# Performance work log

Measured on AMD Instinct MI355X. Metric: run time of the kernel, lower is better.

Reference implementation:

```python
import jax, jax.numpy as jnp
import numpy as np

H, C = 8, 16          # heads, per-head dim; hidden = H*C = 128
NEG_SLOPE = 0.2       # GATConv default
EPS = 1e-5            # GraphNorm eps


def setup_inputs() -> dict:
    key = jax.random.key(0)
    ks = iter(jax.random.split(key, 64))
    Np, Na, D, E = 100000, 50000, 128, 500000
    s = 1.0 / np.sqrt(D)

    def w(shape, scale=1.0):
        return jax.random.normal(next(ks), shape, jnp.float32) * scale

    inp = {
        'x_paper': w((Np, D)),
        'x_author': w((Na, D)),
        'edge_writes': jnp.stack([
            jax.random.randint(next(ks), (E,), 0, Na),
            jax.random.randint(next(ks), (E,), 0, Np)]).astype(jnp.int32),
        'edge_cites': jnp.stack([
            jax.random.randint(next(ks), (E,), 0, Np),
            jax.random.randint(next(ks), (E,), 0, Np)]).astype(jnp.int32),
        'W_lin_paper': w((D, 128), s), 'b_lin_paper': jnp.zeros((128,), jnp.float32),
        'W_lin_author': w((D, 128), s), 'b_lin_author': jnp.zeros((128,), jnp.float32),
        'Wsrc_writes': w((128, 128), s), 'Wdst_writes': w((128, 128), s),
        'atts_writes': w((H, C), 0.1), 'attd_writes': w((H, C), 0.1),
        'bias_writes': jnp.zeros((128,), jnp.float32),
        'Wsrc_cites': w((128, 128), s), 'Wdst_cites': w((128, 128), s),
        'atts_cites': w((H, C), 0.1), 'attd_cites': w((H, C), 0.1),
        'bias_cites': jnp.zeros((128,), jnp.float32),
        'gnw_paper': jnp.ones((128,), jnp.float32), 'gnb_paper': jnp.zeros((128,), jnp.float32),
        'gnm_paper': jnp.ones((128,), jnp.float32),
        'gnw_author': jnp.ones((128,), jnp.float32), 'gnb_author': jnp.zeros((128,), jnp.float32),
        'gnm_author': jnp.ones((128,), jnp.float32),
        'W2_paper': w((128, 128), s), 'b2_paper': jnp.zeros((128,), jnp.float32),
        'W2_author': w((128, 128), s), 'b2_author': jnp.zeros((128,), jnp.float32),
    }
    return inp


def _gat(src_emb, dst_emb, ei, Wsrc, Wdst, att_s, att_d, bias, n_dst):
    # PyG GATConv, bipartite input, concat=True, add_self_loops=True (eval / no dropout)
    n_self = min(src_emb.shape[0], n_dst)
    loops = jnp.arange(n_self, dtype=ei.dtype)
    src = jnp.concatenate([ei[0], loops])
    dst = jnp.concatenate([ei[1], loops])
    xs = (src_emb @ Wsrc).reshape(-1, H, C)          # [Ns,H,C]
    xd = (dst_emb @ Wdst).reshape(-1, H, C)          # [Nd,H,C]
    a_s = (xs * att_s).sum(-1)                       # [Ns,H]
    a_d = (xd * att_d).sum(-1)                       # [Nd,H]
    e = jax.nn.leaky_relu(a_s[src] + a_d[dst], NEG_SLOPE)   # [E,H]
    m = jax.ops.segment_max(e, dst, num_segments=n_dst)
    m = jnp.where(jnp.isfinite(m), m, 0.0)           # guard empty segments
    p = jnp.exp(e - m[dst])
    denom = jax.ops.segment_sum(p, dst, num_segments=n_dst)
    alpha = p / (denom[dst] + 1e-16)                 # segment softmax over dst
    msg = xs[src] * alpha[:, :, None]                # [E,H,C]
    out = jax.ops.segment_sum(msg, dst, num_segments=n_dst)  # [Nd,H,C]
    return out.reshape(n_dst, H * C) + bias


def _gnorm(x, w, b, ms):
    mu = x.mean(0)
    o = x - ms * mu
    var = (o * o).mean(0)
    return w * o * jax.lax.rsqrt(var + EPS) + b


def reference(x_paper, x_author, edge_writes, edge_cites,
              W_lin_paper, b_lin_paper, W_lin_author, b_lin_author,
              Wsrc_writes, Wdst_writes, atts_writes, attd_writes, bias_writes,
              Wsrc_cites, Wdst_cites, atts_cites, attd_cites, bias_cites,
              gnw_paper, gnb_paper, gnm_paper, gnw_author, gnb_author, gnm_author,
              W2_paper, b2_paper, W2_author, b2_author):
    emb_p = jax.nn.relu(x_paper @ W_lin_paper + b_lin_paper)
    emb_a = jax.nn.relu(x_author @ W_lin_author + b_lin_author)
    Np = emb_p.shape[0]
    out_p = _gat(emb_a, emb_p, edge_writes, Wsrc_writes, Wdst_writes,
                 atts_writes, attd_writes, bias_writes, Np)
    out_p = out_p + _gat(emb_p, emb_p, edge_cites, Wsrc_cites, Wdst_cites,
                         atts_cites, attd_cites, bias_cites, Np)
    out_a = jnp.zeros((emb_a.shape[0], H * C), x_author.dtype)  # no edge type targets author
    out_p = _gnorm(out_p, gnw_paper, gnb_paper, gnm_paper) @ W2_paper + b2_paper
    out_a = _gnorm(out_a, gnw_author, gnb_author, gnm_author) @ W2_author + b2_author
    return (out_p, out_a)
```

## Files before the change

### kernel.cpp

```cpp
#include <hip/hip_runtime.h>
#include <cstdint>
#include <cstddef>

#define H 8
#define DHID 128
#define BM 64
#define LDST 136
#define NEG_SLOPE 0.2f
#define GN_EPS 1e-5f

#define SCAN_T 256
#define SCAN_I 4

typedef __attribute__((ext_vector_type(8))) short short8;
typedef __attribute__((ext_vector_type(4))) float f32x4;

__device__ __forceinline__ void atomAddF(float* p, float v) {
    __hip_atomic_fetch_add(p, v, __ATOMIC_RELAXED, __HIP_MEMORY_SCOPE_AGENT);
}
__device__ __forceinline__ unsigned short f2bf(float f) {
    uint32_t u = __float_as_uint(f);
    uint32_t r = (u + 0x7FFFu + ((u >> 16) & 1u)) >> 16;
    return (unsigned short)r;
}
__device__ __forceinline__ uint32_t pack2bf(float lo, float hi) {
    return (uint32_t)f2bf(lo) | ((uint32_t)f2bf(hi) << 16);
}
__device__ __forceinline__ float bflo(uint32_t v) { return __uint_as_float(v << 16); }
__device__ __forceinline__ float bfhi(uint32_t v) { return __uint_as_float(v & 0xFFFF0000u); }

struct PrepHist {
    const float *Wlp, *Wsc, *Wla, *Wsw, *W2p;
    const float *Wdw, *adw, *asc_, *Wdc, *adc_, *asw_;
    unsigned short *WlinP_p, *WsrcP_c, *WlinP_a, *WsrcP_w, *W2P_p, *VscP_p, *VscP_a;
    const float *bw, *bc, *gnb_a, *W2a, *b2a;
    float *bsum, *row_a, *colsum, *colsumsq;
    unsigned short *xs_w_ph, *xs_c_ph;
    float *as_w_ph, *as_c_ph;
    const int *dst_w, *dst_c;
    int *deg, *rank;
    int Ew, Ec, Np, HB0;
};

__global__ void prep_hist(PrepHist a) {
    int b = blockIdx.x, t = threadIdx.x;
    if (b >= a.HB0) {
        int base = (b - a.HB0) * 1024 + t;
        int E = a.Ew + a.Ec;
        int dd[4];
        bool val[4];
#pragma unroll
        for (int j = 0; j < 4; ++j) {
            int i = base + j * 256;
            val[j] = i < E;
            dd[j] = 0;
            if (val[j]) dd[j] = (i < a.Ew) ? a.dst_w[i] : (a.Np + a.dst_c[i - a.Ew]);
        }
        int rk[4];
#pragma unroll
        for (int j = 0; j < 4; ++j)
            if (val[j]) rk[j] = atomicAdd(&a.deg[dd[j]], 1);
#pragma unroll
        for (int j = 0; j < 4; ++j)
            if (val[j]) a.rank[base + j * 256] = rk[j];
        return;
    }
    if (b == 56) {
        if (t < 128) {
            a.bsum[t] = a.bw[t] + a.bc[t];
            float acc = a.b2a[t];
            for (int k = 0; k < DHID; ++k) acc += a.gnb_a[k] * a.W2a[k * DHID + t];
            a.row_a[t] = acc;
            a.colsum[t] = 0.f;
            a.colsumsq[t] = 0.f;
            a.xs_w_ph[t] = 0;
            a.xs_c_ph[t] = 0;
        } else if (t < 136) a.as_w_ph[t - 128] = -1e30f;
        else if (t < 144) a.as_c_ph[t - 136] = -1e30f;
        return;
    }
    int j = b >> 3;
    int idx = (b & 7) * 256 + t;
    int lane = idx & 63, kk = (idx >> 6) & 3, nt = idx >> 8;
    int col = nt * 16 + (lane & 15);
    int k0 = kk * 32 + ((lane >> 4) << 3);
    if (j < 5) {
        const float* W = j == 0 ? a.Wlp : j == 1 ? a.Wsc : j == 2 ? a.Wla : j == 3 ? a.Wsw : a.W2p;
        unsigned short* out = j == 0 ? a.WlinP_p : j == 1 ? a.WsrcP_c : j == 2 ? a.WlinP_a
                              : j == 3 ? a.WsrcP_w : a.W2P_p;
        for (int i = 0; i < 8; ++i) out[idx * 8 + i] = f2bf(W[(k0 + i) * DHID + col]);
    } else if (j == 5) {
        if (idx >= 2 * 256) return;
        const float *W = nullptr, *A = nullptr;
        int h = col & 7;
        if (col < 24) {
            int which = col >> 3;
            W = which == 0 ? a.Wdw : which == 1 ? a.Wsc : a.Wdc;
            A = which == 0 ? a.adw : which == 1 ? a.asc_ : a.adc_;
        }
        for (int i = 0; i < 8; ++i) {
            float v = 0.f;
            if (W)
                for (int c = 0; c < 16; ++c) v += W[(k0 + i) * DHID + h * 16 + c] * A[h * 16 + c];
            a.VscP_p[idx * 8 + i] = f2bf(v);
        }
    } else {
        if (idx >= 256) return;
        int h = col & 7;
        for (int i = 0; i < 8; ++i) {
            float v = 0.f;
            if (col < 8)
                for (int c = 0; c < 16; ++c)
                    v += a.Wsw[(k0 + i) * DHID + h * 16 + c] * a.asw_[h * 16 + c];
            a.VscP_a[idx * 8 + i] = f2bf(v);
        }
    }
}

__global__ void scan1(const int* __restrict__ in, int n, int* __restrict__ out,
                      int* __restrict__ bsums) {
    __shared__ int sh[SCAN_T];
    int t = threadIdx.x;
    long base = (long)blockIdx.x * SCAN_T * SCAN_I;
    int v[SCAN_I];
    int s = 0;
#pragma unroll
    for (int j = 0; j < SCAN_I; ++j) {
        long idx = base + (long)t * SCAN_I + j;
        int x = (idx < n) ? in[idx] : 0;
        x = (x + 3) & ~3;
        v[j] = x;
        s += x;
    }
    sh[t] = s;
    __syncthreads();
    for (int off = 1; off < SCAN_T; off <<= 1) {
        int x = (t >= off) ? sh[t - off] : 0;
        __syncthreads();
        sh[t] += x;
        __syncthreads();
    }
    int run = sh[t] - s;
#pragma unroll
    for (int j = 0; j < SCAN_I; ++j) {
        long idx = base + (long)t * SCAN_I + j;
        if (idx < n) out[idx] = run;
        run += v[j];
    }
    if (t == SCAN_T - 1) bsums[blockIdx.x] = sh[SCAN_T - 1];
}

__global__ void scan3_prefill(const int* __restrict__ off_raw, const int* __restrict__ bs1,
                              int nb, int n2, int* __restrict__ off2,
                              int Np, int Na, int maxTot, int* __restrict__ srcu) {
    __shared__ int pf[SCAN_T];
    int t = threadIdx.x;
    pf[t] = (t < nb) ? bs1[t] : 0;
    __syncthreads();
    for (int off = 1; off < SCAN_T; off <<= 1) {
        int x = (t >= off) ? pf[t - off] : 0;
        __syncthreads();
        pf[t] += x;
        __syncthreads();
    }
    int i = blockIdx.x * 256 + t;
    if (i < n2) {
        int g = i >> 10;
        off2[i] = off_raw[i] + (g ? pf[g - 1] : 0);
    }
    if (blockIdx.x == 0 && t == 0) off2[n2] = pf[nb - 1];
    int gm = Np >> 10;
    int mid = off_raw[Np] + (gm ? pf[gm - 1] : 0);
    long stride = (long)gridDim.x * 256;
    for (long k = i; k < maxTot; k += stride) srcu[k] = (k < (long)mid) ? Na : Np;
}

template <int NSC>
__device__ void proj_body(unsigned short* xt, int bid,
                          const float* __restrict__ x, int nrows,
                          const unsigned short* __restrict__ WlinP, const float* __restrict__ blin,
                          const unsigned short* __restrict__ WsrcP,
                          const unsigned short* __restrict__ VscP,
                          unsigned short* __restrict__ xs,
                          float* __restrict__ a0, float* __restrict__ a1, float* __restrict__ a2) {
    int t = threadIdx.x;
    int lane = t & 63, w = t >> 6;
    long row0 = (long)bid * BM;
    for (int it = 0; it < 16; ++it) {
        int idx2 = t + it * 256;
        int r = idx2 >> 6, cp = idx2 & 63;
        long gr = row0 + r;
        float v0 = 0.f, v1 = 0.f;
        if (gr < nrows) { v0 = x[gr * DHID + 2 * cp]; v1 = x[gr * DHID + 2 * cp + 1]; }
        *reinterpret_cast<uint32_t*>(&xt[r * LDST + 2 * cp]) = pack2bf(v0, v1);
    }
    __syncthreads();
    int arow = w * 16 + (lane & 15);
    int koff = (lane >> 4) << 3;
    short8 af[4];
#pragma unroll
    for (int kk = 0; kk < 4; ++kk)
        af[kk] = *reinterpret_cast<const short8*>(&xt[arow * LDST + kk * 32 + koff]);
    const short8* Bl = reinterpret_cast<const short8*>(WlinP);
    f32x4 acc[8];
#pragma unroll
    for (int nt = 0; nt < 8; ++nt) {
        f32x4 a = {0.f, 0.f, 0.f, 0.f};
#pragma unroll
        for (int kk = 0; kk < 4; ++kk)
            a = __builtin_amdgcn_mfma_f32_16x16x32_bf16(af[kk], Bl[(nt * 4 + kk) * 64 + lane], a, 0, 0, 0);
        acc[nt] = a;
    }
    __syncthreads();
    int orow = w * 16 + ((lane >> 4) << 2);
    int ccol = lane & 15;
#pragma unroll
    for (int nt = 0; nt < 8; ++nt) {
        float b = blin[nt * 16 + ccol];
#pragma unroll
        for (int r = 0; r < 4; ++r) {
            float e = fmaxf(acc[nt][r] + b, 0.f);
            xt[(orow + r) * LDST + nt * 16 + ccol] = f2bf(e);
        }
    }
    __syncthreads();
#pragma unroll
    for (int kk = 0; kk < 4; ++kk)
        af[kk] = *reinterpret_cast<const short8*>(&xt[arow * LDST + kk * 32 + koff]);
    const short8* Bs = reinterpret_cast<const short8*>(WsrcP);
#pragma unroll
    for (int nt = 0; nt < 8; ++nt) {
        f32x4 a = {0.f, 0.f, 0.f, 0.f};
#pragma unroll
        for (int kk = 0; kk < 4; ++kk)
            a = __builtin_amdgcn_mfma_f32_16x16x32_bf16(af[kk], Bs[(nt * 4 + kk) * 64 + lane], a, 0, 0, 0);
        acc[nt] = a;
    }
    const short8* Bv = reinterpret_cast<const short8*>(VscP);
    f32x4 sacc0 = {0.f, 0.f, 0.f, 0.f}, sacc1 = {0.f, 0.f, 0.f, 0.f};
#pragma unroll
    for (int kk = 0; kk < 4; ++kk)
        sacc0 = __builtin_amdgcn_mfma_f32_16x16x32_bf16(af[kk], Bv[kk * 64 + lane], sacc0, 0, 0, 0);
    if (NSC > 1) {
#pragma unroll
        for (int kk = 0; kk < 4; ++kk)
            sacc1 = __builtin_amdgcn_mfma_f32_16x16x32_bf16(af[kk], Bv[(4 + kk) * 64 + lane], sacc1, 0, 0, 0);
    }
#pragma unroll
    for (int nt = 0; nt < 8; ++nt) {
#pragma unroll
        for (int r = 0; r < 4; ++r) {
            long gr = row0 + orow + r;
            if (gr < nrows) xs[gr * DHID + nt * 16 + ccol] = f2bf(acc[nt][r]);
        }
    }
#pragma unroll
    for (int st = 0; st < NSC; ++st) {
        int scol = st * 16 + ccol;
        int h = scol & 7, which = scol >> 3;
        float* ap = which == 0 ? a0 : which == 1 ? a1 : which == 2 ? a2 : nullptr;
        if (ap) {
            f32x4 s = st == 0 ? sacc0 : sacc1;
#pragma unroll
            for (int r = 0; r < 4; ++r) {
                long gr = row0 + orow + r;
                if (gr < nrows) ap[gr * H + h] = s[r];
            }
        }
    }
}

struct MegaArgs {
    const float* x_p; int Np;
    const unsigned short* WlinP_p; const float* blp;
    const unsigned short* WsrcP_c; const unsigned short* VscP_p;
    unsigned short* xs_c; float *a_d_w, *a_s_c, *a_d_c;
    const float* x_a; int Na;
    const unsigned short* WlinP_a; const float* bla;
    const unsigned short* WsrcP_w; const unsigned short* VscP_a;
    unsigned short* xs_w; float* a_s_w;
    const int *src_w, *dst_w, *src_c, *dst_c;
    int Ew, Ec;
    const int *off2, *rank;
    int* srcu;
    int PB, AB;
};

__global__ __launch_bounds__(256) void mega(MegaArgs a) {
    __shared__ unsigned short xt[BM * LDST];
    int b = blockIdx.x;
    if (b < a.PB) {
        proj_body<2>(xt, b, a.x_p, a.Np, a.WlinP_p, a.blp, a.WsrcP_c, a.VscP_p,
                     a.xs_c, a.a_d_w, a.a_s_c, a.a_d_c);
        return;
    }
    if (b < a.PB + a.AB) {
        proj_body<1>(xt, b - a.PB, a.x_a, a.Na, a.WlinP_a, a.bla, a.WsrcP_w, a.VscP_a,
                     a.xs_w, a.a_s_w, nullptr, nullptr);
        return;
    }
    int base = (b - a.PB - a.AB) * 1024 + threadIdx.x;
    int E = a.Ew + a.Ec;
    int s[4], di[4], rk[4];
    bool val[4];
#pragma unroll
    for (int j = 0; j < 4; ++j) {
        int i = base + j * 256;
        val[j] = i < E;
        s[j] = di[j] = rk[j] = 0;
        if (val[j]) {
            if (i < a.Ew) { s[j] = a.src_w[i]; di[j] = a.dst_w[i]; }
            else { int q = i - a.Ew; s[j] = a.src_c[q]; di[j] = a.Np + a.dst_c[q]; }
            rk[j] = a.rank[i];
        }
    }
    int pos[4];
#pragma unroll
    for (int j = 0; j < 4; ++j)
        if (val[j]) pos[j] = a.off2[di[j]] + rk[j];
#pragma unroll
    for (int j = 0; j < 4; ++j)
        if (val[j]) a.srcu[pos[j]] = s[j];
}

#define FILLB 391
__global__ __launch_bounds__(256) void gat_gather(
    const int* __restrict__ off, const int* __restrict__ srcu,
    const float* __restrict__ a_s_w, const float* __restrict__ a_d_w,
    const float* __restrict__ a_s_c, const float* __restrict__ a_d_c,
    const unsigned short* __restrict__ xs_w, const unsigned short* __restrict__ xs_c,
    uint32_t* __restrict__ gatb, int Np, int nselfw,
    const float* __restrict__ row_a, float4* __restrict__ outa, long n4) {
    if (blockIdx.x < FILLB) {
        long i = (long)blockIdx.x * 256 + threadIdx.x;
        long stride = (long)FILLB * 256;
        const float4* r4 = reinterpret_cast<const float4*>(row_a);
        for (; i < n4; i += stride) outa[i] = r4[i & 31];
        return;
    }
    int l = threadIdx.x & 63;
    int d = (blockIdx.x - FILLB) * 4 + (threadIdx.x >> 6);
    if (d >= Np) return;
    int h = l >> 3;
    int iw = off[d], w1 = off[d + 1];
    int ic = off[Np + d], c1 = off[Np + d + 1];
    float adw = a_d_w[(long)d * H + h];
    float adc = a_d_c[(long)d * H + h];
    float denw = 0.f, n0w = 0.f, n1w = 0.f;
    float denc = 0.f, n0c = 0.f, n1c = 0.f;
    if (d < nselfw) {
        float e = a_s_w[(long)d * H + h] + adw;
        e = e > 0.f ? e : NEG_SLOPE * e;
        float p = __expf(e);
        uint32_t v = *reinterpret_cast<const uint32_t*>(xs_w + (long)d * DHID + 2 * l);
        denw += p; n0w += p * bflo(v); n1w += p * bfhi(v);
    }
    {
        float e = a_s_c[(long)d * H + h] + adc;
        e = e > 0.f ? e : NEG_SLOPE * e;
        float p = __expf(e);
        uint32_t v = *reinterpret_cast<const uint32_t*>(xs_c + (long)d * DHID + 2 * l);
        denc += p; n0c += p * bflo(v); n1c += p * bfhi(v);
    }
    while (iw < w1 || ic < c1) {
        bool hw = iw < w1, hc = ic < c1;
        int4 sw, sc;
        if (hw) sw = *reinterpret_cast<const int4*>(srcu + iw);
        if (hc) sc = *reinterpret_cast<const int4*>(srcu + ic);
        float ew[4], ec[4];
        uint32_t vw[4], vc[4];
        if (hw) {
            ew[0] = a_s_w[(long)sw.x * H + h];
            ew[1] = a_s_w[(long)sw.y * H + h];
            ew[2] = a_s_w[(long)sw.z * H + h];
            ew[3] = a_s_w[(long)sw.w * H + h];
            vw[0] = *reinterpret_cast<const uint32_t*>(xs_w + (long)sw.x * DHID + 2 * l);
            vw[1] = *reinterpret_cast<const uint32_t*>(xs_w + (long)sw.y * DHID + 2 * l);
            vw[2] = *reinterpret_cast<const uint32_t*>(xs_w + (long)sw.z * DHID + 2 * l);
            vw[3] = *reinterpret_cast<const uint32_t*>(xs_w + (long)sw.w * DHID + 2 * l);
        }
        if (hc) {
            ec[0] = a_s_c[(long)sc.x * H + h];
            ec[1] = a_s_c[(long)sc.y * H + h];
            ec[2] = a_s_c[(long)sc.z * H + h];
            ec[3] = a_s_c[(long)sc.w * H + h];
            vc[0] = *reinterpret_cast<const uint32_t*>(xs_c + (long)sc.x * DHID + 2 * l);
            vc[1] = *reinterpret_cast<const uint32_t*>(xs_c + (long)sc.y * DHID + 2 * l);
            vc[2] = *reinterpret_cast<const uint32_t*>(xs_c + (long)sc.z * DHID + 2 * l);
            vc[3] = *reinterpret_cast<const uint32_t*>(xs_c + (long)sc.w * DHID + 2 * l);
        }
        if (hw) {
#pragma unroll
            for (int j = 0; j < 4; ++j) {
                float e = ew[j] + adw;
                e = e > 0.f ? e : NEG_SLOPE * e;
                float p = __expf(e);
                denw += p;
                n0w += p * bflo(vw[j]);
                n1w += p * bfhi(vw[j]);
            }
            iw += 4;
        }
        if (hc) {
#pragma unroll
            for (int j = 0; j < 4; ++j) {
                float e = ec[j] + adc;
                e = e > 0.f ? e : NEG_SLOPE * e;
                float p = __expf(e);
                denc += p;
                n0c += p * bflo(vc[j]);
                n1c += p * bfhi(vc[j]);
            }
            ic += 4;
        }
    }
    float rw = 1.f / (denw + 1e-16f);
    float rc = 1.f / (denc + 1e-16f);
    gatb[(long)d * 64 + l] = pack2bf(n0w * rw + n0c * rc, n1w * rw + n1c * rc);
}

#define GN_ROWS 512
__global__ void gn_reduce(const uint32_t* __restrict__ gatb, const float* __restrict__ bsum,
                          float* __restrict__ colsum, float* __restrict__ colsumsq, int Np) {
    int t = threadIdx.x;
    int p = t & 63, ro = t >> 6;
    long r0 = (long)blockIdx.x * GN_ROWS + ro;
    long r1 = min((long)(blockIdx.x + 1) * GN_ROWS, (long)Np);
    float b0 = bsum[2 * p], b1 = bsum[2 * p + 1];
    float s1a = 0.f, s2a = 0.f, s1b = 0.f, s2b = 0.f;
    for (long r = r0; r < r1; r += 4) {
        uint32_t u = gatb[r * 64 + p];
        float x0 = bflo(u) + b0, x1 = bfhi(u) + b1;
        s1a += x0; s2a += x0 * x0;
        s1b += x1; s2b += x1 * x1;
    }
    atomAddF(colsum + 2 * p, s1a);
    atomAddF(colsumsq + 2 * p, s2a);
    atomAddF(colsum + 2 * p + 1, s1b);
    atomAddF(colsumsq + 2 * p + 1, s2b);
}

__global__ __launch_bounds__(256) void final_fill(
    const uint32_t* __restrict__ gatb, const float* __restrict__ bsum,
    const float* __restrict__ colsum, const float* __restrict__ colsumsq,
    const float* __restrict__ gnw, const float* __restrict__ gnb,
    const float* __restrict__ gnm,
    const unsigned short* __restrict__ W2P, const float* __restrict__ b2,
    float* __restrict__ out, int Np) {
    __shared__ unsigned short xt[BM * LDST];
    __shared__ float cscale[DHID], cshift[DHID];
    int b = blockIdx.x;
    int t = threadIdx.x;
    int lane = t & 63, w = t >> 6;
    long row0 = (long)b * BM;
    if (t < DHID) {
        float invN = 1.f / (float)Np;
        float mu = colsum[t] * invN;
        float ms = gnm[t];
        float var = colsumsq[t] * invN - mu * mu * ms * (2.f - ms);
        float sc = gnw[t] * rsqrtf(var + GN_EPS);
        cscale[t] = sc;
        cshift[t] = (bsum[t] - ms * mu) * sc + gnb[t];
    }
    __syncthreads();
    for (int it = 0; it < 16; ++it) {
        int idx2 = t + it * 256;
        int r = idx2 >> 6, cp = idx2 & 63;
        long gr = row0 + r;
        float v0 = 0.f, v1 = 0.f;
        if (gr < Np) {
            uint32_t u = gatb[gr * 64 + cp];
            v0 = bflo(u) * cscale[2 * cp] + cshift[2 * cp];
            v1 = bfhi(u) * cscale[2 * cp + 1] + cshift[2 * cp + 1];
        }
        *reinterpret_cast<uint32_t*>(&xt[r * LDST + 2 * cp]) = pack2bf(v0, v1);
    }
    __syncthreads();
    int arow = w * 16 + (lane & 15);
    int koff = (lane >> 4) << 3;
    short8 af[4];
#pragma unroll
    for (int kk = 0; kk < 4; ++kk)
        af[kk] = *reinterpret_cast<const short8*>(&xt[arow * LDST + kk * 32 + koff]);
    const short8* Bw = reinterpret_cast<const short8*>(W2P);
    int orow = w * 16 + ((lane >> 4) << 2);
    int ccol = lane & 15;
#pragma unroll
    for (int nt = 0; nt < 8; ++nt) {
        f32x4 a = {0.f, 0.f, 0.f, 0.f};
#pragma unroll
        for (int kk = 0; kk < 4; ++kk)
            a = __builtin_amdgcn_mfma_f32_16x16x32_bf16(af[kk], Bw[(nt * 4 + kk) * 64 + lane], a, 0, 0, 0);
        float bb = b2[nt * 16 + ccol];
#pragma unroll
        for (int r = 0; r < 4; ++r) {
            long gr = row0 + orow + r;
            if (gr < Np) out[gr * DHID + nt * 16 + ccol] = a[r] + bb;
        }
    }
}

extern "C" void kernel_launch(void* const* d_in, const int* in_sizes, int n_in,
                              void* d_out, int out_size, void* d_ws, size_t ws_size,
                              hipStream_t stream) {
    const float* x_p   = (const float*)d_in[0];
    const float* x_a   = (const float*)d_in[1];
    const int*   e_w   = (const int*)d_in[2];
    const int*   e_c   = (const int*)d_in[3];
    const float* Wlp   = (const float*)d_in[4];
    const float* blp   = (const float*)d_in[5];
    const float* Wla   = (const float*)d_in[6];
    const float* bla   = (const float*)d_in[7];
    const float* Wsw   = (const float*)d_in[8];
    const float* Wdw   = (const float*)d_in[9];
    const float* asw   = (const float*)d_in[10];
    const float* adw   = (const float*)d_in[11];
    const float* bw    = (const float*)d_in[12];
    const float* Wsc   = (const float*)d_in[13];
    const float* Wdc   = (const float*)d_in[14];
    const float* asc   = (const float*)d_in[15];
    const float* adc   = (const float*)d_in[16];
    const float* bc    = (const float*)d_in[17];
    const float* gnw_p = (const float*)d_in[18];
    const float* gnb_p = (const float*)d_in[19];
    const float* gnm_p = (const float*)d_in[20];
    const float* gnb_a = (const float*)d_in[22];
    const float* W2p   = (const float*)d_in[24];
    const float* b2p   = (const float*)d_in[25];
    const float* W2a   = (const float*)d_in[26];
    const float* b2a   = (const float*)d_in[27];

    int Np = in_sizes[0] / DHID;
    int Na = in_sizes[1] / DHID;
    int Ew = in_sizes[2] / 2;
    int Ec = in_sizes[3] / 2;
    int nself_w = Na < Np ? Na : Np;
    int tot_edges = Ew + Ec;
    int maxTot = tot_edges + 6 * Np + 8;

    float* ws = (float*)d_ws;
    uint32_t* gatb = (uint32_t*)ws;
    float* a_d_w = (float*)(gatb + (size_t)Np * 64);
    float* a_d_c = a_d_w + (size_t)Np * H;
    float* a_s_w = a_d_c + (size_t)Np * H;
    float* a_s_c = a_s_w + (size_t)(Na + 1) * H;
    float* bsum  = a_s_c + (size_t)(Np + 1) * H;
    float* row_a = bsum + DHID;
    float* colsum   = row_a + DHID;
    float* colsumsq = colsum + DHID;
    int*   deg   = (int*)(colsumsq + DHID);
    int* off_raw = deg + 2 * Np;
    int* off2    = off_raw + 2 * Np;
    int* bs1     = off2 + 2 * Np + 1;
    uintptr_t up = (uintptr_t)(bs1 + 512);
    up = (up + 15) & ~(uintptr_t)15;
    int* srcu = (int*)up;
    int* rank = srcu + maxTot;
    unsigned short* xs_w = (unsigned short*)(rank + tot_edges);
    unsigned short* xs_c = xs_w + (size_t)(Na + 1) * DHID;
    up = (uintptr_t)(xs_c + (size_t)(Np + 1) * DHID);
    up = (up + 15) & ~(uintptr_t)15;
    unsigned short* WlinP_p = (unsigned short*)up;
    unsigned short* WsrcP_c = WlinP_p + 16384;
    unsigned short* WlinP_a = WsrcP_c + 16384;
    unsigned short* WsrcP_w = WlinP_a + 16384;
    unsigned short* W2P_p   = WsrcP_w + 16384;
    unsigned short* VscP_p  = W2P_p + 16384;
    unsigned short* VscP_a  = VscP_p + 4096;

    hipMemsetAsync(deg, 0, 2 * (size_t)Np * sizeof(int), stream);

    int HB = (tot_edges + 1023) / 1024;
    {
        PrepHist pa;
        pa.Wlp = Wlp; pa.Wsc = Wsc; pa.Wla = Wla; pa.Wsw = Wsw; pa.W2p = W2p;
        pa.Wdw = Wdw; pa.adw = adw; pa.asc_ = asc; pa.Wdc = Wdc; pa.adc_ = adc; pa.asw_ = asw;
        pa.WlinP_p = WlinP_p; pa.WsrcP_c = WsrcP_c; pa.WlinP_a = WlinP_a;
        pa.WsrcP_w = WsrcP_w; pa.W2P_p = W2P_p; pa.VscP_p = VscP_p; pa.VscP_a = VscP_a;
        pa.bw = bw; pa.bc = bc; pa.gnb_a = gnb_a; pa.W2a = W2a; pa.b2a = b2a;
        pa.bsum = bsum; pa.row_a = row_a; pa.colsum = colsum; pa.colsumsq = colsumsq;
        pa.xs_w_ph = xs_w + (size_t)Na * DHID;
        pa.xs_c_ph = xs_c + (size_t)Np * DHID;
        pa.as_w_ph = a_s_w + (size_t)Na * H;
        pa.as_c_ph = a_s_c + (size_t)Np * H;
        pa.dst_w = e_w + Ew; pa.dst_c = e_c + Ec;
        pa.deg = deg; pa.rank = rank;
        pa.Ew = Ew; pa.Ec = Ec;
        pa.Np = Np; pa.HB0 = 57;
        prep_hist<<<57 + HB, 256, 0, stream>>>(pa);
    }

    int n2 = 2 * Np;
    int nb = (n2 + SCAN_T * SCAN_I - 1) / (SCAN_T * SCAN_I);
    scan1<<<nb, SCAN_T, 0, stream>>>(deg, n2, off_raw, bs1);

    scan3_prefill<<<(maxTot + 255) / 256, 256, 0, stream>>>(
        off_raw, bs1, nb, n2, off2, Np, Na, maxTot, srcu);

    {
        MegaArgs ma;
        ma.x_p = x_p; ma.Np = Np; ma.WlinP_p = WlinP_p; ma.blp = blp;
        ma.WsrcP_c = WsrcP_c; ma.VscP_p = VscP_p;
        ma.xs_c = xs_c; ma.a_d_w = a_d_w; ma.a_s_c = a_s_c; ma.a_d_c = a_d_c;
        ma.x_a = x_a; ma.Na = Na; ma.WlinP_a = WlinP_a; ma.bla = bla;
        ma.WsrcP_w = WsrcP_w; ma.VscP_a = VscP_a;
        ma.xs_w = xs_w; ma.a_s_w = a_s_w;
        ma.src_w = e_w; ma.dst_w = e_w + Ew; ma.src_c = e_c; ma.dst_c = e_c + Ec;
        ma.Ew = Ew; ma.Ec = Ec;
        ma.off2 = off2; ma.rank = rank; ma.srcu = srcu;
        ma.PB = (Np + BM - 1) / BM;
        ma.AB = (Na + BM - 1) / BM;
        int SB = (tot_edges + 1023) / 1024;
        mega<<<ma.PB + ma.AB + SB, 256, 0, stream>>>(ma);
    }

    {
        long n4 = (long)Na * DHID / 4;
        gat_gather<<<FILLB + (Np + 3) / 4, 256, 0, stream>>>(
            off2, srcu, a_s_w, a_d_w, a_s_c, a_d_c, xs_w, xs_c, gatb, Np, nself_w,
            row_a, (float4*)((float*)d_out + (size_t)Np * DHID), n4);
    }

    gn_reduce<<<(Np + GN_ROWS - 1) / GN_ROWS, 256, 0, stream>>>(gatb, bsum, colsum, colsumsq, Np);

    final_fill<<<(Np + BM - 1) / BM, 256, 0, stream>>>(
        gatb, bsum, colsum, colsumsq, gnw_p, gnb_p, gnm_p, W2P_p, b2p,
        (float*)d_out, Np);
}
```

Before: 294.0 us.

## Fill only padded tails of src buffer and make staging wave-local

```diff
diff --git a/kernel.cpp b/kernel.cpp
--- a/kernel.cpp
+++ b/kernel.cpp
@@ -150,9 +150,10 @@
     if (t == SCAN_T - 1) bsums[blockIdx.x] = sh[SCAN_T - 1];
 }
 
-__global__ void scan3_prefill(const int* __restrict__ off_raw, const int* __restrict__ bs1,
-                              int nb, int n2, int* __restrict__ off2,
-                              int Np, int Na, int maxTot, int* __restrict__ srcu) {
+__global__ void scan3_tails(const int* __restrict__ off_raw, const int* __restrict__ bs1,
+                            int nb, int n2, int* __restrict__ off2,
+                            const int* __restrict__ deg,
+                            int Np, int Na, int* __restrict__ srcu) {
     __shared__ int pf[SCAN_T];
     int t = threadIdx.x;
     pf[t] = (t < nb) ? bs1[t] : 0;
@@ -166,13 +167,14 @@
     int i = blockIdx.x * 256 + t;
     if (i < n2) {
         int g = i >> 10;
-        off2[i] = off_raw[i] + (g ? pf[g - 1] : 0);
+        int o = off_raw[i] + (g ? pf[g - 1] : 0);
+        off2[i] = o;
+        int dgi = deg[i];
+        int padded = (dgi + 3) & ~3;
+        int ph = (i < Np) ? Na : Np;
+        for (int k = dgi; k < padded; ++k) srcu[o + k] = ph;
     }
     if (blockIdx.x == 0 && t == 0) off2[n2] = pf[nb - 1];
-    int gm = Np >> 10;
-    int mid = off_raw[Np] + (gm ? pf[gm - 1] : 0);
-    long stride = (long)gridDim.x * 256;
-    for (long k = i; k < maxTot; k += stride) srcu[k] = (k < (long)mid) ? Na : Np;
 }
 
 template <int NSC>
@@ -186,16 +188,15 @@
     int t = threadIdx.x;
     int lane = t & 63, w = t >> 6;
     long row0 = (long)bid * BM;
+    int wrow0 = w * 16;
     for (int it = 0; it < 16; ++it) {
-        int idx2 = t + it * 256;
-        int r = idx2 >> 6, cp = idx2 & 63;
+        int r = wrow0 + it;
         long gr = row0 + r;
         float v0 = 0.f, v1 = 0.f;
-        if (gr < nrows) { v0 = x[gr * DHID + 2 * cp]; v1 = x[gr * DHID + 2 * cp + 1]; }
-        *reinterpret_cast<uint32_t*>(&xt[r * LDST + 2 * cp]) = pack2bf(v0, v1);
-    }
-    __syncthreads();
-    int arow = w * 16 + (lane & 15);
+        if (gr < nrows) { v0 = x[gr * DHID + 2 * lane]; v1 = x[gr * DHID + 2 * lane + 1]; }
+        *reinterpret_cast<uint32_t*>(&xt[r * LDST + 2 * lane]) = pack2bf(v0, v1);
+    }
+    int arow = wrow0 + (lane & 15);
     int koff = (lane >> 4) << 3;
     short8 af[4];
 #pragma unroll
@@ -211,8 +212,7 @@
             a = __builtin_amdgcn_mfma_f32_16x16x32_bf16(af[kk], Bl[(nt * 4 + kk) * 64 + lane], a, 0, 0, 0);
         acc[nt] = a;
     }
-    __syncthreads();
-    int orow = w * 16 + ((lane >> 4) << 2);
+    int orow = wrow0 + ((lane >> 4) << 2);
     int ccol = lane & 15;
 #pragma unroll
     for (int nt = 0; nt < 8; ++nt) {
@@ -223,7 +223,6 @@
             xt[(orow + r) * LDST + nt * 16 + ccol] = f2bf(e);
         }
     }
-    __syncthreads();
 #pragma unroll
     for (int kk = 0; kk < 4; ++kk)
         af[kk] = *reinterpret_cast<const short8*>(&xt[arow * LDST + kk * 32 + koff]);
@@ -463,27 +462,28 @@
         cshift[t] = (bsum[t] - ms * mu) * sc + gnb[t];
     }
     __syncthreads();
+    int wrow0 = w * 16;
+    float cs0 = cscale[2 * lane], cf0 = cshift[2 * lane];
+    float cs1 = cscale[2 * lane + 1], cf1 = cshift[2 * lane + 1];
     for (int it = 0; it < 16; ++it) {
-        int idx2 = t + it * 256;
-        int r = idx2 >> 6, cp = idx2 & 63;
+        int r = wrow0 + it;
         long gr = row0 + r;
         float v0 = 0.f, v1 = 0.f;
         if (gr < Np) {
-            uint32_t u = gatb[gr * 64 + cp];
-            v0 = bflo(u) * cscale[2 * cp] + cshift[2 * cp];
-            v1 = bfhi(u) * cscale[2 * cp + 1] + cshift[2 * cp + 1];
-        }
-        *reinterpret_cast<uint32_t*>(&xt[r * LDST + 2 * cp]) = pack2bf(v0, v1);
-    }
-    __syncthreads();
-    int arow = w * 16 + (lane & 15);
+            uint32_t u = gatb[gr * 64 + lane];
+            v0 = bflo(u) * cs0 + cf0;
+            v1 = bfhi(u) * cs1 + cf1;
+        }
+        *reinterpret_cast<uint32_t*>(&xt[r * LDST + 2 * lane]) = pack2bf(v0, v1);
+    }
+    int arow = wrow0 + (lane & 15);
     int koff = (lane >> 4) << 3;
     short8 af[4];
 #pragma unroll
     for (int kk = 0; kk < 4; ++kk)
         af[kk] = *reinterpret_cast<const short8*>(&xt[arow * LDST + kk * 32 + koff]);
     const short8* Bw = reinterpret_cast<const short8*>(W2P);
-    int orow = w * 16 + ((lane >> 4) << 2);
+    int orow = wrow0 + ((lane >> 4) << 2);
     int ccol = lane & 15;
 #pragma unroll
     for (int nt = 0; nt < 8; ++nt) {
@@ -594,8 +594,8 @@
     int nb = (n2 + SCAN_T * SCAN_I - 1) / (SCAN_T * SCAN_I);
     scan1<<<nb, SCAN_T, 0, stream>>>(deg, n2, off_raw, bs1);
 
-    scan3_prefill<<<(maxTot + 255) / 256, 256, 0, stream>>>(
-        off_raw, bs1, nb, n2, off2, Np, Na, maxTot, srcu);
+    scan3_tails<<<(n2 + 255) / 256, 256, 0, stream>>>(
+        off_raw, bs1, nb, n2, off2, deg, Np, Na, srcu);
 
     {
         MegaArgs ma;
```

Result: no change. 297.3 us (+1.1%).
